# Kernel tuning notes

Hardware: AMD Instinct MI355X
Metric: run time of the kernel (lower is better)

## Reference

```python
import jax, jax.numpy as jnp
import numpy as np

# config mirroring init_kwargs
PPD = (64, 64)                      # points_per_dim (spatial grid)
GRID_RANGE = ((-1.0, 1.0), (-1.0, 1.0))
B, N, NT, DX, DZ = 2, 2048, 8, 3, 16
INIT_LS = 0.1
TIME_DIM = 0


def construct_grid():
    axes = [jnp.linspace(lo, hi, p, dtype=jnp.float32) for (lo, hi), p in zip(GRID_RANGE, PPD)]
    mesh = jnp.meshgrid(*axes, indexing='ij')
    return jnp.stack(mesh, axis=-1)  # (H, W, 2)


def setup_inputs() -> dict:
    key = jax.random.key(0)
    k1, k2, k3 = jax.random.split(key, 3)
    x = jax.random.uniform(k1, (B, N, DX), jnp.float32, -1.0, 1.0)
    z = jax.random.normal(k2, (B, N, DZ), jnp.float32)
    time_grid = jnp.sort(jax.random.uniform(k3, (B, NT), jnp.float32, -1.0, 1.0), axis=-1)
    # raw parameter s.t. softplus(param) == INIT_LS (inverse-softplus init)
    lengthscale_param = jnp.full((DX,), float(np.log(np.exp(INIT_LS) - 1.0)), jnp.float32)
    return {"x": x, "z": z, "time_grid": time_grid, "lengthscale_param": lengthscale_param}


def reference(x, z, time_grid, lengthscale_param):
    H, W = PPD
    b = x.shape[0]
    t = time_grid.shape[1]
    grid = construct_grid()  # (H, W, 2)

    ls = 1e-5 + jax.nn.softplus(lengthscale_param)  # (DX,)

    # x_grid: [b, t, H, W, DX] with the time coordinate at coord index TIME_DIM(=0)
    spatial = jnp.broadcast_to(grid, (b, t, H, W, 2))
    tg = jnp.broadcast_to(time_grid[:, :, None, None, None], (b, t, H, W, 1))
    x_grid = jnp.concatenate([tg, spatial], axis=-1)

    G = t * H * W
    xg_flat = x_grid.reshape(b, G, DX)

    # pre_exp[b, g, n] = sum_d (xg - x)^2 / ls_d^2, computed via scaled-coordinate
    # norm expansion to avoid materializing the [b, G, n, DX] difference tensor.
    a = xg_flat / ls                          # [b, G, DX]
    c = x / ls                                # [b, n, DX]
    pre_exp = (jnp.sum(a * a, axis=-1)[:, :, None]
               + jnp.sum(c * c, axis=-1)[:, None, :]
               - 2.0 * jnp.einsum('bgd,bnd->bgn', a, c))
    weights = jnp.exp(-0.5 * pre_exp)         # [b, G, n]  (RBF weights)

    z_grid = jnp.einsum('bgn,bne->bge', weights, z)  # [b, G, DZ]
    z_grid = z_grid.reshape(b, t, H, W, DZ)
    return x_grid, z_grid
```

## Files before the change

kernel.cpp:

```cpp
#include <hip/hip_runtime.h>
#include <math.h>

#define B_  2
#define N_  2048
#define NT_ 8
#define DZ_ 16
#define H_  64
#define W_  64

#define XGRID_SIZE (B_*NT_*H_*W_*3)
#define CUT 12.0f
#define CH  128

using half8   = __attribute__((ext_vector_type(8))) _Float16;
using floatx4 = __attribute__((ext_vector_type(4))) float;

__global__ __launch_bounds__(256, 4) void fused_kernel(
    const float* __restrict__ x,
    const float* __restrict__ z,
    const float* __restrict__ tg,
    const float* __restrict__ lsp,
    float* __restrict__ out)
{
    const int i    = blockIdx.x & 63;
    const int t    = (blockIdx.x >> 6) & 7;
    const int b    = blockIdx.x >> 9;
    const int tid  = threadIdx.x;
    const int w    = tid >> 6;
    const int lane = tid & 63;
    const int quad = lane >> 4;
    const int col  = lane & 15;

    const float step = 2.0f / 63.0f;
    const float C    = 0.84932180f;

    const float r0 = C / (1e-5f + log1pf(expf(lsp[0])));
    const float r1 = C / (1e-5f + log1pf(expf(lsp[1])));
    const float r2 = C / (1e-5f + log1pf(expf(lsp[2])));

    const float tval = tg[b*NT_ + t];
    const float gi   = -1.0f + step * (float)i;

    union REDU {
        float2 cuc[N_ + CH];
        float  red[4][64][DZ_ + 1];
    };
    __shared__ REDU sm;
    __shared__ int  cidx[N_ + CH];
    __shared__ int  s_cnt;

    if (tid == 0) s_cnt = 0;
    __syncthreads();

    const float* __restrict__ xb = x + b*N_*3;
    for (int k0 = 0; k0 < N_; k0 += 256) {
        int k = k0 + tid;
        float x0 = xb[k*3 + 0];
        float x1 = xb[k*3 + 1];
        float x2 = xb[k*3 + 2];
        float dt = (tval - x0) * r0;
        float di = (gi   - x1) * r1;
        float sq = fmaf(dt, dt, di*di);
        bool keep = (sq < CUT);
        unsigned long long mb = __ballot(keep);
        int cnt = __popcll(mb);
        int base = 0;
        if (lane == 0) base = atomicAdd(&s_cnt, cnt);
        base = __shfl(base, 0, 64);
        if (keep) {
            int rank = __popcll(mb & ((1ull << lane) - 1ull));
            int pos  = base + rank;
            sm.cuc[pos] = make_float2(sq, x2 * r2);
            cidx[pos]   = k;
        }
    }

    if (tid < 192) {
        int jj = tid / 3;
        int c  = tid - jj*3;
        float gj = -1.0f + step * (float)jj;
        float v  = (c == 0) ? tval : ((c == 1) ? gi : gj);
        out[(size_t)blockIdx.x * 192 + tid] = v;
    }

    __syncthreads();
    const int M = s_cnt;
    if (tid < CH) {
        sm.cuc[M + tid] = make_float2(1e9f, 0.f);
        cidx[M + tid]   = 0;
    }
    __syncthreads();

    const int NC = (M + CH - 1) / CH;

    const float* __restrict__ zb = z + b*N_*DZ_;
    const int koff = w*32 + (quad << 3);

    const float aj0 = (-1.0f + step * (float)( 0 + col)) * r2;
    const float aj1 = (-1.0f + step * (float)(16 + col)) * r2;
    const float aj2 = (-1.0f + step * (float)(32 + col)) * r2;
    const float aj3 = (-1.0f + step * (float)(48 + col)) * r2;

    floatx4 acc0 = {0.f,0.f,0.f,0.f};
    floatx4 acc1 = {0.f,0.f,0.f,0.f};
    floatx4 acc2 = {0.f,0.f,0.f,0.f};
    floatx4 acc3 = {0.f,0.f,0.f,0.f};

    float zreg[8];
    {
        int idx[8];
        #pragma unroll
        for (int jj = 0; jj < 8; ++jj) idx[jj] = cidx[koff + jj];
        #pragma unroll
        for (int jj = 0; jj < 8; ++jj)
            zreg[jj] = zb[(size_t)idx[jj] * DZ_ + col];
    }

    for (int c = 0; c < NC; ++c) {
        half8 bf;
        #pragma unroll
        for (int jj = 0; jj < 8; ++jj) bf[jj] = (_Float16)zreg[jj];

        const int base = c*CH + koff;
        float2 mm[8];
        #pragma unroll
        for (int jj = 0; jj < 8; ++jj) mm[jj] = sm.cuc[base + jj];

        if (c + 1 < NC) {
            const int base2 = (c + 1)*CH + koff;
            int idx[8];
            #pragma unroll
            for (int jj = 0; jj < 8; ++jj) idx[jj] = cidx[base2 + jj];
            #pragma unroll
            for (int jj = 0; jj < 8; ++jj)
                zreg[jj] = zb[(size_t)idx[jj] * DZ_ + col];
        }

        half8 a0, a1, a2, a3;
        #pragma unroll
        for (int jj = 0; jj < 8; ++jj) {
            float s  = mm[jj].x;
            float cx = mm[jj].y;
            float d0 = aj0 - cx;
            float d1 = aj1 - cx;
            float d2 = aj2 - cx;
            float d3 = aj3 - cx;
            a0[jj] = (_Float16)exp2f(-fmaf(d0, d0, s));
            a1[jj] = (_Float16)exp2f(-fmaf(d1, d1, s));
            a2[jj] = (_Float16)exp2f(-fmaf(d2, d2, s));
            a3[jj] = (_Float16)exp2f(-fmaf(d3, d3, s));
        }

        acc0 = __builtin_amdgcn_mfma_f32_16x16x32_f16(a0, bf, acc0, 0, 0, 0);
        acc1 = __builtin_amdgcn_mfma_f32_16x16x32_f16(a1, bf, acc1, 0, 0, 0);
        acc2 = __builtin_amdgcn_mfma_f32_16x16x32_f16(a2, bf, acc2, 0, 0, 0);
        acc3 = __builtin_amdgcn_mfma_f32_16x16x32_f16(a3, bf, acc3, 0, 0, 0);
    }

    __syncthreads();

    #pragma unroll
    for (int r = 0; r < 4; ++r) sm.red[w][ 0 + quad*4 + r][col] = acc0[r];
    #pragma unroll
    for (int r = 0; r < 4; ++r) sm.red[w][16 + quad*4 + r][col] = acc1[r];
    #pragma unroll
    for (int r = 0; r < 4; ++r) sm.red[w][32 + quad*4 + r][col] = acc2[r];
    #pragma unroll
    for (int r = 0; r < 4; ++r) sm.red[w][48 + quad*4 + r][col] = acc3[r];
    __syncthreads();

    const int jj = tid >> 2;
    const int eg = (tid & 3) * 4;
    float4 s4 = make_float4(0.f, 0.f, 0.f, 0.f);
    #pragma unroll
    for (int ww = 0; ww < 4; ++ww) {
        s4.x += sm.red[ww][jj][eg + 0];
        s4.y += sm.red[ww][jj][eg + 1];
        s4.z += sm.red[ww][jj][eg + 2];
        s4.w += sm.red[ww][jj][eg + 3];
    }
    float* og = out + XGRID_SIZE + (size_t)blockIdx.x * (W_ * DZ_);
    *(float4*)(og + jj*DZ_ + eg) = s4;
}

extern "C" void kernel_launch(void* const* d_in, const int* in_sizes, int n_in,
                              void* d_out, int out_size, void* d_ws, size_t ws_size,
                              hipStream_t stream) {
    const float* x   = (const float*)d_in[0];
    const float* z   = (const float*)d_in[1];
    const float* tg  = (const float*)d_in[2];
    const float* lsp = (const float*)d_in[3];

    float* out = (float*)d_out;

    fused_kernel<<<1024, 256, 0, stream>>>(x, z, tg, lsp, out);
}
```

Before: 72.76 us.

## Pre-cull points by time distance in a separate kernel before the fused pass

Adds a small prepass kernel that, for each (batch, time) pair, keeps only points whose scaled time distance falls under the cutoff. It writes them compactly to workspace as float4 records holding the scaled coords, squared time distance and index. The main kernel then scans only this shorter list instead of all points, which cuts global loads and per-point arithmetic in its culling phase. The cost is an extra kernel launch, a serial dependency between the two kernels, and workspace traffic.

```diff
diff --git a/kernel.cpp b/kernel.cpp
--- a/kernel.cpp
+++ b/kernel.cpp
@@ -15,16 +15,69 @@
 using half8   = __attribute__((ext_vector_type(8))) _Float16;
 using floatx4 = __attribute__((ext_vector_type(4))) float;
 
+
+__global__ __launch_bounds__(1024) void tcull_kernel(
+    const float* __restrict__ x,
+    const float* __restrict__ tg,
+    const float* __restrict__ lsp,
+    float4* __restrict__ wsl,
+    int* __restrict__ wcnt)
+{
+    const int bt   = blockIdx.x;
+    const int b    = bt >> 3;
+    const int t    = bt & 7;
+    const int tid  = threadIdx.x;
+    const int lane = tid & 63;
+
+    const float C = 0.84932180f;
+    const float r0 = C / (1e-5f + log1pf(expf(lsp[0])));
+    const float r1 = C / (1e-5f + log1pf(expf(lsp[1])));
+    const float r2 = C / (1e-5f + log1pf(expf(lsp[2])));
+
+    const float tval = tg[b*NT_ + t];
+
+    __shared__ int s_cnt;
+    if (tid == 0) s_cnt = 0;
+    __syncthreads();
+
+    const float* __restrict__ xb = x + b*N_*3;
+    float4* __restrict__ outl = wsl + (size_t)bt * N_;
+
+    for (int k0 = 0; k0 < N_; k0 += 1024) {
+        int k = k0 + tid;
+        float x0 = xb[k*3 + 0];
+        float x1 = xb[k*3 + 1];
+        float x2 = xb[k*3 + 2];
+        float dt  = (tval - x0) * r0;
+        float dt2 = dt * dt;
+        bool keep = (dt2 < CUT);
+        unsigned long long mb = __ballot(keep);
+        int cnt = __popcll(mb);
+        int base = 0;
+        if (lane == 0) base = atomicAdd(&s_cnt, cnt);
+        base = __shfl(base, 0, 64);
+        if (keep) {
+            int rank = __popcll(mb & ((1ull << lane) - 1ull));
+            outl[base + rank] =
+                make_float4(x1 * r1, x2 * r2, dt2, __int_as_float(k));
+        }
+    }
+    __syncthreads();
+    if (tid == 0) wcnt[bt] = s_cnt;
+}
+
 __global__ __launch_bounds__(256, 4) void fused_kernel(
-    const float* __restrict__ x,
     const float* __restrict__ z,
     const float* __restrict__ tg,
     const float* __restrict__ lsp,
+    const float4* __restrict__ wsl,
+    const int* __restrict__ wcnt,
     float* __restrict__ out)
 {
     const int i    = blockIdx.x & 63;
     const int t    = (blockIdx.x >> 6) & 7;
     const int b    = blockIdx.x >> 9;
+    const int bt   = b*NT_ + t;
     const int tid  = threadIdx.x;
     const int w    = tid >> 6;
     const int lane = tid & 63;
@@ -34,12 +87,12 @@
     const float step = 2.0f / 63.0f;
     const float C    = 0.84932180f;
 
-    const float r0 = C / (1e-5f + log1pf(expf(lsp[0])));
     const float r1 = C / (1e-5f + log1pf(expf(lsp[1])));
     const float r2 = C / (1e-5f + log1pf(expf(lsp[2])));
 
-    const float tval = tg[b*NT_ + t];
+    const float tval = tg[bt];
     const float gi   = -1.0f + step * (float)i;
+    const float gir1 = gi * r1;
 
     union REDU {
         float2 cuc[N_ + CH];
@@ -47,21 +100,26 @@
     };
     __shared__ REDU sm;
     __shared__ int  cidx[N_ + CH];
-    __shared__ int  s_cnt;
-
-    if (tid == 0) s_cnt = 0;
-    __syncthreads();
-
-    const float* __restrict__ xb = x + b*N_*3;
-    for (int k0 = 0; k0 < N_; k0 += 256) {
+    __shared__ int  s_cnt, s_Mt;
+
+    if (tid == 0) { s_cnt = 0; s_Mt = wcnt[bt]; }
+    __syncthreads();
+    const int Mt = s_Mt;
+
+    const float4* __restrict__ lst = wsl + (size_t)bt * N_;
+    for (int k0 = 0; k0 < Mt; k0 += 256) {
         int k = k0 + tid;
-        float x0 = xb[k*3 + 0];
-        float x1 = xb[k*3 + 1];
-        float x2 = xb[k*3 + 2];
-        float dt = (tval - x0) * r0;
-        float di = (gi   - x1) * r1;
-        float sq = fmaf(dt, dt, di*di);
-        bool keep = (sq < CUT);
+        bool keep = false;
+        float sq = 0.f, cx = 0.f;
+        int   n  = 0;
+        if (k < Mt) {
+            float4 f = lst[k];
+            float di = gir1 - f.x;
+            sq = fmaf(di, di, f.z);
+            cx = f.y;
+            n  = __float_as_int(f.w);
+            keep = (sq < CUT);
+        }
         unsigned long long mb = __ballot(keep);
         int cnt = __popcll(mb);
         int base = 0;
@@ -70,8 +128,8 @@
         if (keep) {
             int rank = __popcll(mb & ((1ull << lane) - 1ull));
             int pos  = base + rank;
-            sm.cuc[pos] = make_float2(sq, x2 * r2);
-            cidx[pos]   = k;
+            sm.cuc[pos] = make_float2(sq, cx);
+            cidx[pos]   = n;
         }
     }
 
@@ -193,5 +251,9 @@
 
     float* out = (float*)d_out;
 
-    fused_kernel<<<1024, 256, 0, stream>>>(x, z, tg, lsp, out);
+    float4* wsl  = (float4*)d_ws;
+    int*    wcnt = (int*)((char*)d_ws + (size_t)16 * N_ * sizeof(float4));
+
+    tcull_kernel<<<16, 1024, 0, stream>>>(x, tg, lsp, wsl, wcnt);
+    fused_kernel<<<1024, 256, 0, stream>>>(z, tg, lsp, wsl, wcnt, out);
 }
```

Result: slower. 75.53 us (+3.8%).

## Pre-bucket points by time cutoff and x1 to shrink per-block candidate scan

Applied to the files above, without the earlier changes.

Adds a preliminary kernel that, per (batch, time) pair, filters points by the time-distance cutoff and counting-sorts the survivors into 64 buckets along the x1 coordinate, writing a compact list plus bucket offsets to workspace. The main kernel then reads only the bucket range that can fall within the cutoff for its grid row, instead of scanning all 2048 points with a ballot/atomic compaction. This cuts the redundant per-block filtering over N, at the cost of a second launch, workspace traffic, and a slightly looser candidate set (whole buckets) that adds a few extra MFMA chunks.

```diff
diff --git a/kernel.cpp b/kernel.cpp
--- a/kernel.cpp
+++ b/kernel.cpp
@@ -11,20 +11,99 @@
 #define XGRID_SIZE (B_*NT_*H_*W_*3)
 #define CUT 12.0f
 #define CH  128
+#define NBUK 64
+#define SCAP 1024
 
 using half8   = __attribute__((ext_vector_type(8))) _Float16;
 using floatx4 = __attribute__((ext_vector_type(4))) float;
 
+
+__global__ __launch_bounds__(1024) void sort_kernel(
+    const float* __restrict__ x,
+    const float* __restrict__ tg,
+    const float* __restrict__ lsp,
+    float4* __restrict__ wsl,
+    int* __restrict__ woff)
+{
+    const int bt  = blockIdx.x;
+    const int b   = bt >> 3;
+    const int tid = threadIdx.x;
+
+    const float C  = 0.84932180f;
+    const float r0 = C / (1e-5f + log1pf(expf(lsp[0])));
+    const float r1 = C / (1e-5f + log1pf(expf(lsp[1])));
+    const float r2 = C / (1e-5f + log1pf(expf(lsp[2])));
+
+    const float tval = tg[bt];
+
+    __shared__ int hist[NBUK];
+    __shared__ int offs[NBUK + 1];
+    __shared__ int cur[NBUK];
+
+    if (tid < NBUK) hist[tid] = 0;
+    __syncthreads();
+
+    const float* __restrict__ xb = x + b*N_*3;
+
+    float sx1[2], sx2[2], sdt2[2];
+    int   sbuk[2], skey[2];
+    bool  skeep[2];
+    #pragma unroll
+    for (int r = 0; r < 2; ++r) {
+        int k = r*1024 + tid;
+        float x0 = xb[k*3 + 0];
+        float x1 = xb[k*3 + 1];
+        float x2 = xb[k*3 + 2];
+        float dt  = (tval - x0) * r0;
+        float dt2 = dt * dt;
+        bool keep = (dt2 < CUT);
+        int buk = (int)((x1 + 1.0f) * (NBUK * 0.5f));
+        buk = min(max(buk, 0), NBUK - 1);
+        skeep[r] = keep; sbuk[r] = buk; skey[r] = k;
+        sx1[r] = x1 * r1; sx2[r] = x2 * r2; sdt2[r] = dt2;
+        if (keep) atomicAdd(&hist[buk], 1);
+    }
+    __syncthreads();
+
+    if (tid < NBUK) {
+        int h = hist[tid];
+        int v = h;
+        #pragma unroll
+        for (int d = 1; d < NBUK; d <<= 1) {
+            int u = __shfl_up(v, d, 64);
+            if (tid >= d) v += u;
+        }
+        offs[tid + 1] = v;
+        cur[tid] = v - h;
+        if (tid == 0) offs[0] = 0;
+    }
+    __syncthreads();
+
+    float4* __restrict__ outl = wsl + (size_t)bt * N_;
+    #pragma unroll
+    for (int r = 0; r < 2; ++r) {
+        if (skeep[r]) {
+            int pos = atomicAdd(&cur[sbuk[r]], 1);
+            outl[pos] = make_float4(sx1[r], sx2[r], sdt2[r],
+                                    __int_as_float(skey[r]));
+        }
+    }
+    __syncthreads();
+    if (tid <= NBUK) woff[bt*(NBUK+1) + tid] = offs[tid];
+}
+
 __global__ __launch_bounds__(256, 4) void fused_kernel(
-    const float* __restrict__ x,
     const float* __restrict__ z,
     const float* __restrict__ tg,
     const float* __restrict__ lsp,
+    const float4* __restrict__ wsl,
+    const int* __restrict__ woff,
     float* __restrict__ out)
 {
     const int i    = blockIdx.x & 63;
     const int t    = (blockIdx.x >> 6) & 7;
     const int b    = blockIdx.x >> 9;
+    const int bt   = b*NT_ + t;
     const int tid  = threadIdx.x;
     const int w    = tid >> 6;
     const int lane = tid & 63;
@@ -34,46 +113,27 @@
     const float step = 2.0f / 63.0f;
     const float C    = 0.84932180f;
 
-    const float r0 = C / (1e-5f + log1pf(expf(lsp[0])));
     const float r1 = C / (1e-5f + log1pf(expf(lsp[1])));
     const float r2 = C / (1e-5f + log1pf(expf(lsp[2])));
 
-    const float tval = tg[b*NT_ + t];
+    const float tval = tg[bt];
     const float gi   = -1.0f + step * (float)i;
-
-    union REDU {
-        float2 cuc[N_ + CH];
-        float  red[4][64][DZ_ + 1];
+    const float gir1 = gi * r1;
+
+    const float wid = sqrtf(CUT) / r1;
+    int lob = (int)floorf((gi - wid + 1.0f) * (NBUK * 0.5f));
+    int hib = (int)floorf((gi + wid + 1.0f) * (NBUK * 0.5f));
+    lob = min(max(lob, 0), NBUK - 1);
+    hib = min(max(hib, 0), NBUK - 1);
+    const int lo = woff[bt*(NBUK+1) + lob];
+    const int hi = woff[bt*(NBUK+1) + hib + 1];
+    const int Mr = hi - lo;
+
+    union SM {
+        struct { float2 cuc[SCAP + CH]; int cidx[SCAP + CH]; } c;
+        float red[4][64][DZ_ + 1];
     };
-    __shared__ REDU sm;
-    __shared__ int  cidx[N_ + CH];
-    __shared__ int  s_cnt;
-
-    if (tid == 0) s_cnt = 0;
-    __syncthreads();
-
-    const float* __restrict__ xb = x + b*N_*3;
-    for (int k0 = 0; k0 < N_; k0 += 256) {
-        int k = k0 + tid;
-        float x0 = xb[k*3 + 0];
-        float x1 = xb[k*3 + 1];
-        float x2 = xb[k*3 + 2];
-        float dt = (tval - x0) * r0;
-        float di = (gi   - x1) * r1;
-        float sq = fmaf(dt, dt, di*di);
-        bool keep = (sq < CUT);
-        unsigned long long mb = __ballot(keep);
-        int cnt = __popcll(mb);
-        int base = 0;
-        if (lane == 0) base = atomicAdd(&s_cnt, cnt);
-        base = __shfl(base, 0, 64);
-        if (keep) {
-            int rank = __popcll(mb & ((1ull << lane) - 1ull));
-            int pos  = base + rank;
-            sm.cuc[pos] = make_float2(sq, x2 * r2);
-            cidx[pos]   = k;
-        }
-    }
+    __shared__ SM sm;
 
     if (tid < 192) {
         int jj = tid / 3;
@@ -83,17 +143,8 @@
         out[(size_t)blockIdx.x * 192 + tid] = v;
     }
 
-    __syncthreads();
-    const int M = s_cnt;
-    if (tid < CH) {
-        sm.cuc[M + tid] = make_float2(1e9f, 0.f);
-        cidx[M + tid]   = 0;
-    }
-    __syncthreads();
-
-    const int NC = (M + CH - 1) / CH;
-
-    const float* __restrict__ zb = z + b*N_*DZ_;
+    const float* __restrict__ zb  = z + b*N_*DZ_;
+    const float4* __restrict__ lst = wsl + (size_t)bt * N_;
     const int koff = w*32 + (quad << 3);
 
     const float aj0 = (-1.0f + step * (float)( 0 + col)) * r2;
@@ -106,55 +157,82 @@
     floatx4 acc2 = {0.f,0.f,0.f,0.f};
     floatx4 acc3 = {0.f,0.f,0.f,0.f};
 
-    float zreg[8];
-    {
-        int idx[8];
-        #pragma unroll
-        for (int jj = 0; jj < 8; ++jj) idx[jj] = cidx[koff + jj];
-        #pragma unroll
-        for (int jj = 0; jj < 8; ++jj)
-            zreg[jj] = zb[(size_t)idx[jj] * DZ_ + col];
-    }
-
-    for (int c = 0; c < NC; ++c) {
-        half8 bf;
-        #pragma unroll
-        for (int jj = 0; jj < 8; ++jj) bf[jj] = (_Float16)zreg[jj];
-
-        const int base = c*CH + koff;
-        float2 mm[8];
-        #pragma unroll
-        for (int jj = 0; jj < 8; ++jj) mm[jj] = sm.cuc[base + jj];
-
-        if (c + 1 < NC) {
-            const int base2 = (c + 1)*CH + koff;
+    int nst = (Mr + SCAP - 1) / SCAP;
+    if (nst < 1) nst = 1;
+
+    for (int st = 0; st < nst; ++st) {
+        const int sbase = lo + st * SCAP;
+        int cnt = hi - sbase;
+        cnt = min(cnt, SCAP);
+        cnt = max(cnt, 0);
+
+        if (st > 0) __syncthreads();
+
+        for (int k = tid; k < cnt; k += 256) {
+            float4 f = lst[sbase + k];
+            float di = gir1 - f.x;
+            sm.c.cuc[k]  = make_float2(fmaf(di, di, f.z), f.y);
+            sm.c.cidx[k] = __float_as_int(f.w);
+        }
+        const int cpad = (cnt + CH - 1) & ~(CH - 1);
+        for (int k = cnt + tid; k < cpad; k += 256) {
+            sm.c.cuc[k]  = make_float2(1e9f, 0.f);
+            sm.c.cidx[k] = 0;
+        }
+        __syncthreads();
+
+        const int NC = cpad >> 7;
+
+        float zreg[8];
+        if (NC > 0) {
             int idx[8];
             #pragma unroll
-            for (int jj = 0; jj < 8; ++jj) idx[jj] = cidx[base2 + jj];
+            for (int jj = 0; jj < 8; ++jj) idx[jj] = sm.c.cidx[koff + jj];
             #pragma unroll
             for (int jj = 0; jj < 8; ++jj)
                 zreg[jj] = zb[(size_t)idx[jj] * DZ_ + col];
         }
 
-        half8 a0, a1, a2, a3;
-        #pragma unroll
-        for (int jj = 0; jj < 8; ++jj) {
-            float s  = mm[jj].x;
-            float cx = mm[jj].y;
-            float d0 = aj0 - cx;
-            float d1 = aj1 - cx;
-            float d2 = aj2 - cx;
-            float d3 = aj3 - cx;
-            a0[jj] = (_Float16)exp2f(-fmaf(d0, d0, s));
-            a1[jj] = (_Float16)exp2f(-fmaf(d1, d1, s));
-            a2[jj] = (_Float16)exp2f(-fmaf(d2, d2, s));
-            a3[jj] = (_Float16)exp2f(-fmaf(d3, d3, s));
-        }
-
-        acc0 = __builtin_amdgcn_mfma_f32_16x16x32_f16(a0, bf, acc0, 0, 0, 0);
-        acc1 = __builtin_amdgcn_mfma_f32_16x16x32_f16(a1, bf, acc1, 0, 0, 0);
-        acc2 = __builtin_amdgcn_mfma_f32_16x16x32_f16(a2, bf, acc2, 0, 0, 0);
-        acc3 = __builtin_amdgcn_mfma_f32_16x16x32_f16(a3, bf, acc3, 0, 0, 0);
+        for (int c = 0; c < NC; ++c) {
+            half8 bf;
+            #pragma unroll
+            for (int jj = 0; jj < 8; ++jj) bf[jj] = (_Float16)zreg[jj];
+
+            const int base = c*CH + koff;
+            float2 mm[8];
+            #pragma unroll
+            for (int jj = 0; jj < 8; ++jj) mm[jj] = sm.c.cuc[base + jj];
+
+            if (c + 1 < NC) {
+                const int base2 = (c + 1)*CH + koff;
+                int idx[8];
+                #pragma unroll
+                for (int jj = 0; jj < 8; ++jj) idx[jj] = sm.c.cidx[base2 + jj];
+                #pragma unroll
+                for (int jj = 0; jj < 8; ++jj)
+                    zreg[jj] = zb[(size_t)idx[jj] * DZ_ + col];
+            }
+
+            half8 a0, a1, a2, a3;
+            #pragma unroll
+            for (int jj = 0; jj < 8; ++jj) {
+                float s  = mm[jj].x;
+                float cx = mm[jj].y;
+                float d0 = aj0 - cx;
+                float d1 = aj1 - cx;
+                float d2 = aj2 - cx;
+                float d3 = aj3 - cx;
+                a0[jj] = (_Float16)exp2f(-fmaf(d0, d0, s));
+                a1[jj] = (_Float16)exp2f(-fmaf(d1, d1, s));
+                a2[jj] = (_Float16)exp2f(-fmaf(d2, d2, s));
+                a3[jj] = (_Float16)exp2f(-fmaf(d3, d3, s));
+            }
+
+            acc0 = __builtin_amdgcn_mfma_f32_16x16x32_f16(a0, bf, acc0, 0, 0, 0);
+            acc1 = __builtin_amdgcn_mfma_f32_16x16x32_f16(a1, bf, acc1, 0, 0, 0);
+            acc2 = __builtin_amdgcn_mfma_f32_16x16x32_f16(a2, bf, acc2, 0, 0, 0);
+            acc3 = __builtin_amdgcn_mfma_f32_16x16x32_f16(a3, bf, acc3, 0, 0, 0);
+        }
     }
 
     __syncthreads();
@@ -193,5 +271,9 @@
 
     float* out = (float*)d_out;
 
-    fused_kernel<<<1024, 256, 0, stream>>>(x, z, tg, lsp, out);
+    float4* wsl  = (float4*)d_ws;
+    int*    woff = (int*)((char*)d_ws + (size_t)16 * N_ * sizeof(float4));
+
+    sort_kernel<<<16, 1024, 0, stream>>>(x, tg, lsp, wsl, woff);
+    fused_kernel<<<1024, 256, 0, stream>>>(z, tg, lsp, wsl, woff, out);
 }
```

Result: slower. 74.71 us (+2.7%).
